# Kernel optimization log

Measured on AMD Instinct MI355X. Metric: run time of the kernel, lower is better.

The kernel has to match this reference:

```python
import jax, jax.numpy as jnp
import numpy as np

N = 50000
E = 800000
IN_F = 128
OUT_F = 128


def setup_inputs() -> dict:
    key = jax.random.key(0)
    k1, k2, k3, k4, k5 = jax.random.split(key, 5)
    x = jax.random.normal(k1, (N, IN_F), dtype=jnp.float32)
    # sparse adjacency as COO edge list: row = dst (aggregating node), col = src
    edge_index = jax.random.randint(k2, (2, E), 0, N, dtype=jnp.int64)
    edge_weight = jax.random.uniform(k3, (E,), dtype=jnp.float32)
    # nn.Linear(in_features, out_features): W is [out, in], b is [out]
    W = jax.random.normal(k4, (OUT_F, IN_F), dtype=jnp.float32) * (1.0 / np.sqrt(IN_F))
    b = jax.random.normal(k5, (OUT_F,), dtype=jnp.float32) * 0.01
    return {"x": x, "edge_index": edge_index, "edge_weight": edge_weight, "W": W, "b": b}


def reference(x, edge_index, edge_weight, W, b):
    # hidden = self.linear(x)  -> [N, out]
    hidden = jnp.einsum("ni,oi->no", x, W) + b
    # out = adj @ hidden (SpMM): out[dst] += w_e * hidden[src]
    dst = edge_index[0]
    src = edge_index[1]
    msgs = edge_weight[:, None] * hidden[src]  # [E, out]
    out = jax.ops.segment_sum(msgs, dst, num_segments=x.shape[0])
    return out
```

## Files before the change

kernel.cpp:

```cpp
#include <hip/hip_runtime.h>
#include <hip/hip_bf16.h>

#define N_NODES 50000
#define N_EDGES 800000
#define FEAT    128
#define N_TILES (N_NODES / 16)
#define GEMM_BLOCKS 784
#define MAXD    32
#define OVF_CAP 16384
#define NODES_PER_GRP 6250
#define CHUNK   2048
#define NCHUNK  ((N_EDGES + CHUNK - 1) / CHUNK)
#define QCAP    110000
#define SCAT_BPG 98

using short8  = __attribute__((ext_vector_type(8))) short;
using float4v = __attribute__((ext_vector_type(4))) float;


__device__ __forceinline__ unsigned short f2b(float f) {
    __hip_bfloat16 h = __float2bfloat16(f);
    return __builtin_bit_cast(unsigned short, h);
}

__global__ __launch_bounds__(256) void k_fused(const float* __restrict__ x,
                                               const float* __restrict__ W,
                                               const float* __restrict__ bias,
                                               unsigned short* __restrict__ hidden,
                                               const int* __restrict__ ei,
                                               const float* __restrict__ wt,
                                               int* __restrict__ flag,
                                               int2* __restrict__ queue) {
    __shared__ __align__(16) unsigned short Wlds[128 * 136];
    const int t = threadIdx.x;

    if (blockIdx.x < GEMM_BLOCKS) {
        for (int j = 0; j < 16; ++j) {
            int idx4 = j * 256 + t;
            float4v wv = *(const float4v*)(W + (size_t)idx4 * 4);
            int r = (idx4 * 4) >> 7;
            int c = (idx4 * 4) & 127;
            unsigned short* p = &Wlds[r * 136 + c];
            p[0] = f2b(wv[0]); p[1] = f2b(wv[1]); p[2] = f2b(wv[2]); p[3] = f2b(wv[3]);
        }
        __syncthreads();

        const int wave = t >> 6;
        const int lane = t & 63;
        int tile = blockIdx.x * 4 + wave;
        if (tile >= N_TILES) tile = N_TILES - 1;
        const int rowBase = tile * 16;
        const int m    = lane & 15;
        const int quad = lane >> 4;

        float4v acc[8];
        #pragma unroll
        for (int i = 0; i < 8; ++i) acc[i] = (float4v){0.f, 0.f, 0.f, 0.f};

        #pragma unroll
        for (int kk = 0; kk < 4; ++kk) {
            const int k0 = kk * 32 + quad * 8;
            const float* ap = x + (size_t)(rowBase + m) * FEAT + k0;
            float4v a0 = *(const float4v*)(ap);
            float4v a1 = *(const float4v*)(ap + 4);
            short8 af;
            #pragma unroll
            for (int j = 0; j < 4; ++j) { af[j] = (short)f2b(a0[j]); af[4 + j] = (short)f2b(a1[j]); }
            #pragma unroll
            for (int nt = 0; nt < 8; ++nt) {
                short8 bf = *(const short8*)&Wlds[(nt * 16 + m) * 136 + k0];
                acc[nt] = __builtin_amdgcn_mfma_f32_16x16x32_bf16(af, bf, acc[nt], 0, 0, 0);
            }
        }

        const int r0 = rowBase + quad * 4;
        #pragma unroll
        for (int nt = 0; nt < 8; ++nt) {
            const int col = nt * 16 + m;
            const float bc = bias[col];
            #pragma unroll
            for (int r = 0; r < 4; ++r) {
                hidden[(size_t)(r0 + r) * FEAT + col] = f2b(acc[nt][r] + bc);
            }
        }
    } else {
        int* lcnt  = (int*)Wlds;
        int* gbase = lcnt + 8;
        const int bid  = blockIdx.x - GEMM_BLOCKS;
        const int lane = t & 63;

        unsigned long long mball = __ballot(ei[2 * lane + 1] != 0);
        const int sh = (mball == 0ULL) ? 1 : 0;

        if (t < 8) lcnt[t] = 0;
        __syncthreads();

        const int e0 = bid * CHUNK + t;
        int      dstv[8];
        unsigned recv_[8];
        int      lpos[8];
        #pragma unroll
        for (int i = 0; i < 8; ++i) {
            int e = e0 + i * 256;
            if (e < N_EDGES) {
                int dst = ei[(size_t)e << sh];
                if ((unsigned)dst >= N_NODES) dst = 0;
                int src = ei[(size_t)(N_EDGES + e) << sh];
                if ((unsigned)src >= N_NODES) src = 0;
                dstv[i]  = dst;
                recv_[i] = ((unsigned)f2b(wt[e]) << 16) | (unsigned)src;
                lpos[i]  = atomicAdd(&lcnt[dst / NODES_PER_GRP], 1);
            } else {
                dstv[i] = -1;
            }
        }
        __syncthreads();
        if (t < 8) gbase[t] = atomicAdd(&flag[16 + 16 * t], lcnt[t]);
        __syncthreads();

        #pragma unroll
        for (int i = 0; i < 8; ++i) {
            if (dstv[i] < 0) continue;
            int g   = dstv[i] / NODES_PER_GRP;
            int idx = gbase[g] + lpos[i];
            if (idx < QCAP) {
                int2 r; r.x = dstv[i]; r.y = (int)recv_[i];
                queue[(size_t)g * QCAP + idx] = r;
            }
        }
    }
}

__global__ __launch_bounds__(256) void k_scat(const int2* __restrict__ queue,
                                              int* __restrict__ flag,
                                              int* __restrict__ fill,
                                              unsigned int* __restrict__ slots,
                                              int2* __restrict__ ovf) {
    const int g = blockIdx.x & 7;
    const int b = blockIdx.x >> 3;
    int n = flag[16 + 16 * g]; if (n > QCAP) n = QCAP;
    const int2* q = queue + (size_t)g * QCAP;

    for (int i = b * 256 + (int)threadIdx.x; i < n; i += SCAT_BPG * 256) {
        int2 ent = q[i];
        int dst = ent.x;
        int pos = atomicAdd(&fill[dst], 1);
        if (pos < MAXD) {
            slots[(size_t)dst * MAXD + pos] = (unsigned int)ent.y;
        } else {
            int op = atomicAdd(&flag[1], 1);
            if (op < OVF_CAP) { int2 r; r.x = dst; r.y = ent.y; ovf[op] = r; }
        }
    }
}

#define AGG_FMA(w_, h_)                                                      \
    acc[0] = fmaf(w_, __uint_as_float((h_.x & 0xffffu) << 16), acc[0]);      \
    acc[1] = fmaf(w_, __uint_as_float(h_.x & 0xffff0000u),     acc[1]);      \
    acc[2] = fmaf(w_, __uint_as_float((h_.y & 0xffffu) << 16), acc[2]);      \
    acc[3] = fmaf(w_, __uint_as_float(h_.y & 0xffff0000u),     acc[3]);      \
    acc[4] = fmaf(w_, __uint_as_float((h_.z & 0xffffu) << 16), acc[4]);      \
    acc[5] = fmaf(w_, __uint_as_float(h_.z & 0xffff0000u),     acc[5]);      \
    acc[6] = fmaf(w_, __uint_as_float((h_.w & 0xffffu) << 16), acc[6]);      \
    acc[7] = fmaf(w_, __uint_as_float(h_.w & 0xffff0000u),     acc[7]);

__global__ __launch_bounds__(256) void k_agg(const int* __restrict__ fill,
                                             const unsigned int* __restrict__ slots,
                                             const unsigned int* __restrict__ hid,
                                             const int* __restrict__ flag,
                                             const int2* __restrict__ ovf,
                                             float* __restrict__ out) {
    const int wave = threadIdx.x >> 6;
    const int lane = threadIdx.x & 63;
    const int node = blockIdx.x * 4 + wave;
    const int grp  = lane >> 4;
    const int sub  = lane & 15;

    const int degf = fill[node];
    const int deg  = (degf > MAXD) ? MAXD : degf;
    const uint4* sl4 = (const uint4*)(slots + (size_t)node * MAXD);

    float acc[8];
    #pragma unroll
    for (int j = 0; j < 8; ++j) acc[j] = 0.f;

    const int iters = (deg + 3) >> 2;
    for (int it = 0; it < iters; it += 4) {
        uint4 r0 = sl4[it];
        uint4 r1 = sl4[(it + 1) & 7];
        uint4 r2 = sl4[(it + 2) & 7];
        uint4 r3 = sl4[(it + 3) & 7];
        unsigned rc0 = (grp < 2) ? (grp == 0 ? r0.x : r0.y) : (grp == 2 ? r0.z : r0.w);
        unsigned rc1 = (grp < 2) ? (grp == 0 ? r1.x : r1.y) : (grp == 2 ? r1.z : r1.w);
        unsigned rc2 = (grp < 2) ? (grp == 0 ? r2.x : r2.y) : (grp == 2 ? r2.z : r2.w);
        unsigned rc3 = (grp < 2) ? (grp == 0 ? r3.x : r3.y) : (grp == 2 ? r3.z : r3.w);
        const int e0 = it * 4 + grp;
        const bool v0 = (e0)      < deg;
        const bool v1 = (e0 + 4)  < deg;
        const bool v2 = (e0 + 8)  < deg;
        const bool v3 = (e0 + 12) < deg;
        const float w0 = v0 ? __uint_as_float(rc0 & 0xffff0000u) : 0.f;
        const float w1 = v1 ? __uint_as_float(rc1 & 0xffff0000u) : 0.f;
        const float w2 = v2 ? __uint_as_float(rc2 & 0xffff0000u) : 0.f;
        const float w3 = v3 ? __uint_as_float(rc3 & 0xffff0000u) : 0.f;
        const unsigned s0 = v0 ? (rc0 & 0xffffu) : 0u;
        const unsigned s1 = v1 ? (rc1 & 0xffffu) : 0u;
        const unsigned s2 = v2 ? (rc2 & 0xffffu) : 0u;
        const unsigned s3 = v3 ? (rc3 & 0xffffu) : 0u;
        uint4 h0 = *((const uint4*)(hid + (size_t)s0 * 64) + sub);
        uint4 h1 = *((const uint4*)(hid + (size_t)s1 * 64) + sub);
        uint4 h2 = *((const uint4*)(hid + (size_t)s2 * 64) + sub);
        uint4 h3 = *((const uint4*)(hid + (size_t)s3 * 64) + sub);
        AGG_FMA(w0, h0)
        AGG_FMA(w1, h1)
        AGG_FMA(w2, h2)
        AGG_FMA(w3, h3)
    }

    if (degf > MAXD) {
        int n = flag[1]; if (n > OVF_CAP) n = OVF_CAP;
        for (int i = 0; i < n; ++i) {
            int2 r = ovf[i];
            if (r.x != node || (i & 3) != grp) continue;
            unsigned rec = (unsigned)r.y;
            float w = __uint_as_float(rec & 0xffff0000u);
            unsigned src = rec & 0xffffu;
            uint4 h = *((const uint4*)(hid + (size_t)src * 64) + sub);
            AGG_FMA(w, h)
        }
    }

    #pragma unroll
    for (int j = 0; j < 8; ++j) {
        float a = acc[j];
        a += __shfl_xor(a, 16, 64);
        a += __shfl_xor(a, 32, 64);
        acc[j] = a;
    }

    if (lane < 16) {
        float* o = out + (size_t)node * FEAT + sub * 8;
        *(float4*)(o)     = make_float4(acc[0], acc[1], acc[2], acc[3]);
        *(float4*)(o + 4) = make_float4(acc[4], acc[5], acc[6], acc[7]);
    }
}

extern "C" void kernel_launch(void* const* d_in, const int* in_sizes, int n_in,
                              void* d_out, int out_size, void* d_ws, size_t ws_size,
                              hipStream_t stream) {
    const float* x  = (const float*)d_in[0];
    const int*   ei = (const int*)d_in[1];
    const float* ew = (const float*)d_in[2];
    const float* W  = (const float*)d_in[3];
    const float* b  = (const float*)d_in[4];
    float* out = (float*)d_out;

    int*  flag = (int*)d_ws;
    int*  fill = flag + 256;
    int2* ovf  = (int2*)(fill + 50048);
    unsigned int* slots = (unsigned int*)(ovf + OVF_CAP);
    unsigned short* hidden = (unsigned short*)(slots + (size_t)N_NODES * MAXD);
    int2* queue = (int2*)(hidden + (size_t)N_NODES * FEAT);

    hipMemsetAsync(d_ws, 0, 256 * sizeof(int) + 50048 * sizeof(int), stream);

    k_fused<<<GEMM_BLOCKS + NCHUNK, 256, 0, stream>>>(x, W, b, hidden, ei, ew,
                                                      flag, queue);
    k_scat <<<8 * SCAT_BPG, 256, 0, stream>>>(queue, flag, fill, slots, ovf);
    k_agg  <<<N_NODES / 4, 256, 0, stream>>>(fill, slots, (const unsigned int*)hidden,
                                             flag, ovf, out);
}
```

Before: 166.3 us.

## Pre-convert W to bf16 in a prep kernel and drop LDS staging

Adds a small prep kernel that zeroes the workspace counters, replacing the memset, and converts W to bf16 once in global memory. The GEMM blocks no longer stage and convert W into a 34 KB LDS tile per block with a barrier. Instead each wave loads B fragments directly from the bf16 W in global memory, which should hit in cache. This cuts per-block setup work and LDS use, allowing more blocks per CU, at the cost of an extra launch and global/L2 reads for B.

```diff
diff --git a/kernel.cpp b/kernel.cpp
--- a/kernel.cpp
+++ b/kernel.cpp
@@ -23,28 +23,34 @@
     return __builtin_bit_cast(unsigned short, h);
 }
 
+__global__ __launch_bounds__(256) void k_prep(const float* __restrict__ W,
+                                              int* __restrict__ ws_ints,
+                                              unsigned short* __restrict__ wbf) {
+    const int gid = blockIdx.x * 256 + threadIdx.x;
+    if (gid < 12576) ((int4*)ws_ints)[gid] = make_int4(0, 0, 0, 0);
+    if (gid < 2048) {
+        const float* s = W + (size_t)gid * 8;
+        float4v a0 = *(const float4v*)(s);
+        float4v a1 = *(const float4v*)(s + 4);
+        short8 v;
+        #pragma unroll
+        for (int j = 0; j < 4; ++j) { v[j] = (short)f2b(a0[j]); v[4 + j] = (short)f2b(a1[j]); }
+        *(short8*)(wbf + (size_t)gid * 8) = v;
+    }
+}
+
 __global__ __launch_bounds__(256) void k_fused(const float* __restrict__ x,
-                                               const float* __restrict__ W,
+                                               const unsigned short* __restrict__ wbf,
                                                const float* __restrict__ bias,
                                                unsigned short* __restrict__ hidden,
                                                const int* __restrict__ ei,
                                                const float* __restrict__ wt,
                                                int* __restrict__ flag,
                                                int2* __restrict__ queue) {
-    __shared__ __align__(16) unsigned short Wlds[128 * 136];
+    __shared__ int pshared[16];
     const int t = threadIdx.x;
 
     if (blockIdx.x < GEMM_BLOCKS) {
-        for (int j = 0; j < 16; ++j) {
-            int idx4 = j * 256 + t;
-            float4v wv = *(const float4v*)(W + (size_t)idx4 * 4);
-            int r = (idx4 * 4) >> 7;
-            int c = (idx4 * 4) & 127;
-            unsigned short* p = &Wlds[r * 136 + c];
-            p[0] = f2b(wv[0]); p[1] = f2b(wv[1]); p[2] = f2b(wv[2]); p[3] = f2b(wv[3]);
-        }
-        __syncthreads();
-
         const int wave = t >> 6;
         const int lane = t & 63;
         int tile = blockIdx.x * 4 + wave;
@@ -57,19 +63,24 @@
         #pragma unroll
         for (int i = 0; i < 8; ++i) acc[i] = (float4v){0.f, 0.f, 0.f, 0.f};
 
+        short8 af[4];
         #pragma unroll
         for (int kk = 0; kk < 4; ++kk) {
             const int k0 = kk * 32 + quad * 8;
             const float* ap = x + (size_t)(rowBase + m) * FEAT + k0;
             float4v a0 = *(const float4v*)(ap);
             float4v a1 = *(const float4v*)(ap + 4);
-            short8 af;
             #pragma unroll
-            for (int j = 0; j < 4; ++j) { af[j] = (short)f2b(a0[j]); af[4 + j] = (short)f2b(a1[j]); }
+            for (int j = 0; j < 4; ++j) { af[kk][j] = (short)f2b(a0[j]); af[kk][4 + j] = (short)f2b(a1[j]); }
+        }
+
+        #pragma unroll
+        for (int nt = 0; nt < 8; ++nt) {
+            const unsigned short* wrow = wbf + (size_t)(nt * 16 + m) * FEAT + quad * 8;
             #pragma unroll
-            for (int nt = 0; nt < 8; ++nt) {
-                short8 bf = *(const short8*)&Wlds[(nt * 16 + m) * 136 + k0];
-                acc[nt] = __builtin_amdgcn_mfma_f32_16x16x32_bf16(af, bf, acc[nt], 0, 0, 0);
+            for (int kk = 0; kk < 4; ++kk) {
+                short8 bf = *(const short8*)(wrow + kk * 32);
+                acc[nt] = __builtin_amdgcn_mfma_f32_16x16x32_bf16(af[kk], bf, acc[nt], 0, 0, 0);
             }
         }
 
@@ -84,8 +95,8 @@
             }
         }
     } else {
-        int* lcnt  = (int*)Wlds;
-        int* gbase = lcnt + 8;
+        int* lcnt  = pshared;
+        int* gbase = pshared + 8;
         const int bid  = blockIdx.x - GEMM_BLOCKS;
         const int lane = t & 63;
 
@@ -261,10 +272,10 @@
     unsigned int* slots = (unsigned int*)(ovf + OVF_CAP);
     unsigned short* hidden = (unsigned short*)(slots + (size_t)N_NODES * MAXD);
     int2* queue = (int2*)(hidden + (size_t)N_NODES * FEAT);
-
-    hipMemsetAsync(d_ws, 0, 256 * sizeof(int) + 50048 * sizeof(int), stream);
-
-    k_fused<<<GEMM_BLOCKS + NCHUNK, 256, 0, stream>>>(x, W, b, hidden, ei, ew,
+    unsigned short* wbf = (unsigned short*)(queue + (size_t)8 * QCAP);
+
+    k_prep <<<64, 256, 0, stream>>>(W, flag, wbf);
+    k_fused<<<GEMM_BLOCKS + NCHUNK, 256, 0, stream>>>(x, wbf, b, hidden, ei, ew,
                                                       flag, queue);
     k_scat <<<8 * SCAT_BPG, 256, 0, stream>>>(queue, flag, fill, slots, ovf);
     k_agg  <<<N_NODES / 4, 256, 0, stream>>>(fill, slots, (const unsigned int*)hidden,
```

Measured after the change: 178.2 us. 7.2% more time.
